# Kernel optimization log

Hardware: AMD Instinct MI355X
Metric: run time of the kernel (lower is better)

## Reference

```python
import jax, jax.numpy as jnp
import numpy as np
from jax import lax


def setup_inputs() -> dict:
    key = jax.random.key(0)
    t_in = jax.random.normal(key, (16, 65536, 3), dtype=jnp.float32)
    return {"npoints": 2048, "t_in": t_in}


def reference(npoints, t_in):
    """Iterative farthest point sampling.

    t_in: (b, n, 3) float32 point coordinates.
    Returns (b, npoints) int32 indices of sampled points.
    Matches the PointNet++ CUDA kernel semantics: first sample is index 0,
    running min-distance buffer initialized to a large value, each step
    picks the argmax of the min-distance to the already-selected set.
    """
    b, n, p = t_in.shape
    assert p == 3
    BIG = jnp.float32(1e10)

    batch_ix = jnp.arange(b)

    def step(carry, _):
        dist, last_idx = carry                      # dist: (b,n), last_idx: (b,)
        last = t_in[batch_ix, last_idx]             # (b,3) last selected points
        d = jnp.sum((t_in - last[:, None, :]) ** 2, axis=-1)  # (b,n)
        dist = jnp.minimum(dist, d)
        nxt = jnp.argmax(dist, axis=-1).astype(jnp.int32)      # (b,)
        return (dist, nxt), nxt

    init_idx = jnp.zeros((b,), dtype=jnp.int32)
    dist0 = jnp.full((b, n), BIG, dtype=jnp.float32)
    (_, _), idxs = lax.scan(step, (dist0, init_idx), None, length=npoints - 1)
    # idxs: (npoints-1, b) -> (b, npoints-1)
    out = jnp.concatenate([init_idx[:, None], idxs.T], axis=1)  # (b, npoints)
    return out
```

## Files before the change

kernel.cpp:

```cpp
#include <hip/hip_runtime.h>
#include <stdint.h>


#define NBATCH   16
#define NPTS     65536
#define NPOINTS  2048
#define KBLK     16
#define THREADS  256
#define WPB      64
#define PPB      4096
#define PPT      16
#define SLOT_U64 8
#define REGION_U64 (WPB * SLOT_U64)

#define TAGOK(w) (((unsigned)((w) >> 16) & 0xFFFFu) == tag)

typedef unsigned int uint4v __attribute__((ext_vector_type(4)));

__device__ __forceinline__ void load_slot16(const unsigned long long* p,
                                            unsigned long long& w0,
                                            unsigned long long& w1) {
    uint4v r;
    asm volatile("global_load_dwordx4 %0, %1, off sc0 sc1\n\t"
                 "s_waitcnt vmcnt(0)"
                 : "=v"(r) : "v"(p) : "memory");
    w0 = ((unsigned long long)r.y << 32) | r.x;
    w1 = ((unsigned long long)r.w << 32) | r.z;
}

__global__ __launch_bounds__(THREADS, 1)
void fps_kernel(const float* __restrict__ pts, int* __restrict__ out,
                unsigned long long* __restrict__ slots)
{
    const int bid  = blockIdx.x;
    const int g    = bid & 15;
    const int blk  = bid >> 4;
    const int tid  = threadIdx.x;
    const int lane = tid & 63;
    const int wave = tid >> 6;
    const int widx = (blk << 2) + wave;

    const float* __restrict__ P = pts + (size_t)g * (NPTS * 3);

    __shared__ unsigned long long s_flag[2];

    float  x[PPT], y[PPT], z[PPT];
    double dist[PPT];
    const int base = blk * PPB;
#pragma unroll
    for (int j = 0; j < PPT; ++j) {
        const int idx = base + j * THREADS + tid;
        x[j] = P[idx * 3 + 0];
        y[j] = P[idx * 3 + 1];
        z[j] = P[idx * 3 + 2];
        dist[j] = 1e10;
    }
    if (tid == 0) { s_flag[0] = 0ull; s_flag[1] = 0ull; }
    __syncthreads();

    double qx = (double)P[0], qy = (double)P[1], qz = (double)P[2];
    if (blk == 0 && tid == 0) out[g * NPOINTS] = 0;

    for (int it = 0; it < NPOINTS - 1; ++it) {
        double bd = -1.0;
        int    bi = 0x7FFFFFFF;
        {
#pragma clang fp contract(off)
#pragma unroll
            for (int j = 0; j < PPT; ++j) {
                const double dx = (double)x[j] - qx;
                const double dy = (double)y[j] - qy;
                const double dz = (double)z[j] - qz;
                const double d  = (dx * dx + dy * dy) + dz * dz;
                const double nd = fmin(dist[j], d);
                dist[j] = nd;
                const bool t = nd > bd;
                bd = t ? nd : bd;
                bi = t ? (base + j * THREADS + tid) : bi;
            }
        }

#pragma unroll
        for (int m = 1; m < 64; m <<= 1) {
            const double od = __shfl_xor(bd, m, 64);
            const int    oi = __shfl_xor(bi, m, 64);
            const bool t = (od > bd) || (od == bd && oi < bi);
            bd = t ? od : bd; bi = t ? oi : bi;
        }

        const unsigned tag = (unsigned)(it + 1);
        const int par = it & 1;
        unsigned long long* rb =
            slots + (size_t)(par * NBATCH + g) * REGION_U64;

        {
            const unsigned long long B =
                (unsigned long long)__double_as_longlong(bd);
            const unsigned long long TI =
                  ((unsigned long long)tag << 16)
                | (unsigned long long)((unsigned)bi & 0xFFFFu);
            const unsigned long long hi32 =
                (lane == 0) ? (B >> 32) : (B & 0xFFFFFFFFull);
            if (lane < 2) {
                __hip_atomic_store(rb + widx * SLOT_U64 + lane,
                                   (hi32 << 32) | TI,
                                   __ATOMIC_RELAXED, __HIP_MEMORY_SCOPE_AGENT);
            }
        }

        int wi;
        if (wave == 0) {
            unsigned long long* sp = rb + lane * SLOT_U64;
            __builtin_amdgcn_s_sleep(4);
            unsigned long long l0 = 0, l1 = 0;
            bool ok = false;
            int g1 = 0;
            do {
                load_slot16(sp, l0, l1);
                ok = TAGOK(l0) & TAGOK(l1);
            } while (!ok && ++g1 < 32);
            int g2 = 0;
            while (!ok) {
                l0 = __hip_atomic_load(sp + 0, __ATOMIC_RELAXED,
                                       __HIP_MEMORY_SCOPE_AGENT);
                l1 = __hip_atomic_load(sp + 1, __ATOMIC_RELAXED,
                                       __HIP_MEMORY_SCOPE_AGENT);
                ok = TAGOK(l0) & TAGOK(l1);
                if (++g2 > (1 << 20)) break;
            }

            double cd = __longlong_as_double(
                (long long)(((l0 >> 32) << 32) | (l1 >> 32)));
            int    ci = (int)(l0 & 0xFFFFull);

#pragma unroll
            for (int m = 1; m < 64; m <<= 1) {
                const double od = __shfl_xor(cd, m, 64);
                const int    oi = __shfl_xor(ci, m, 64);
                const bool t = (od > cd) || (od == cd && oi < ci);
                cd = t ? od : cd; ci = t ? oi : ci;
            }

            if (lane == 0) {
                __hip_atomic_store(&s_flag[par],
                                   ((unsigned long long)(unsigned)ci << 32)
                                 | (unsigned long long)tag,
                                   __ATOMIC_RELAXED,
                                   __HIP_MEMORY_SCOPE_WORKGROUP);
                if (blk == 0) out[g * NPOINTS + it + 1] = ci;
            }
            wi = ci;
        } else {
            unsigned long long fv;
            int guard = 0;
            do {
                fv = __hip_atomic_load(&s_flag[par], __ATOMIC_RELAXED,
                                       __HIP_MEMORY_SCOPE_WORKGROUP);
            } while (((unsigned)fv != tag) && ++guard < (1 << 20));
            wi = (int)(fv >> 32);
        }

        const float* pw = P + (size_t)(unsigned)wi * 3;
        qx = (double)pw[0]; qy = (double)pw[1]; qz = (double)pw[2];
    }
}

extern "C" void kernel_launch(void* const* d_in, const int* in_sizes, int n_in,
                              void* d_out, int out_size, void* d_ws, size_t ws_size,
                              hipStream_t stream) {
    (void)in_sizes; (void)n_in; (void)out_size; (void)ws_size;
    const float* t_in = (const float*)d_in[1];
    int* out = (int*)d_out;
    unsigned long long* slots = (unsigned long long*)d_ws;

    dim3 grid(NBATCH * KBLK);
    dim3 block(THREADS);
    void* args[] = { (void*)&t_in, (void*)&out, (void*)&slots };
    hipLaunchCooperativeKernel((const void*)fps_kernel, grid, block, args, 0, stream);
}
```

Before: 5.079 ms.

## Reduce per-block wave candidates in LDS before cross-block global exchange

Waves 1-3 now publish their per-wave best candidate to shared memory, and wave 0 merges them with its own before writing a single slot per block to global memory. The global exchange region shrinks from 64 wave slots to 16 block slots, so the poller reads fewer lines and runs a shorter shuffle reduction. In exchange, wave 0 must spin on LDS for the other waves before publishing, which adds a serial intra-block step to the critical path of every iteration.

Result: faster. 4.839 ms (-4.7%).

```diff
diff --git a/kernel.cpp b/kernel.cpp
--- a/kernel.cpp
+++ b/kernel.cpp
@@ -7,11 +7,10 @@
 #define NPOINTS  2048
 #define KBLK     16
 #define THREADS  256
-#define WPB      64
 #define PPB      4096
 #define PPT      16
 #define SLOT_U64 8
-#define REGION_U64 (WPB * SLOT_U64)
+#define REGION_U64 (KBLK * SLOT_U64)
 
 #define TAGOK(w) (((unsigned)((w) >> 16) & 0xFFFFu) == tag)
 
@@ -38,11 +37,11 @@
     const int tid  = threadIdx.x;
     const int lane = tid & 63;
     const int wave = tid >> 6;
-    const int widx = (blk << 2) + wave;
 
     const float* __restrict__ P = pts + (size_t)g * (NPTS * 3);
 
     __shared__ unsigned long long s_flag[2];
+    __shared__ unsigned long long s_cand[2][3][2];
 
     float  x[PPT], y[PPT], z[PPT];
     double dist[PPT];
@@ -55,7 +54,10 @@
         z[j] = P[idx * 3 + 2];
         dist[j] = 1e10;
     }
-    if (tid == 0) { s_flag[0] = 0ull; s_flag[1] = 0ull; }
+    if (tid < 16) {
+        ((unsigned long long*)s_cand)[tid & 11] = 0ull;
+        if (tid < 2) s_flag[tid] = 0ull;
+    }
     __syncthreads();
 
     double qx = (double)P[0], qy = (double)P[1], qz = (double)P[2];
@@ -93,24 +95,75 @@
         unsigned long long* rb =
             slots + (size_t)(par * NBATCH + g) * REGION_U64;
 
-        {
-            const unsigned long long B =
-                (unsigned long long)__double_as_longlong(bd);
-            const unsigned long long TI =
-                  ((unsigned long long)tag << 16)
-                | (unsigned long long)((unsigned)bi & 0xFFFFu);
-            const unsigned long long hi32 =
-                (lane == 0) ? (B >> 32) : (B & 0xFFFFFFFFull);
-            if (lane < 2) {
-                __hip_atomic_store(rb + widx * SLOT_U64 + lane,
-                                   (hi32 << 32) | TI,
-                                   __ATOMIC_RELAXED, __HIP_MEMORY_SCOPE_AGENT);
-            }
-        }
-
         int wi;
-        if (wave == 0) {
-            unsigned long long* sp = rb + lane * SLOT_U64;
+        if (wave != 0) {
+            if (lane == 0) {
+                const unsigned long long B =
+                    (unsigned long long)__double_as_longlong(bd);
+                const unsigned long long TI =
+                      ((unsigned long long)tag << 16)
+                    | (unsigned long long)((unsigned)bi & 0xFFFFu);
+                __hip_atomic_store(&s_cand[par][wave - 1][0],
+                                   ((B >> 32) << 32) | TI,
+                                   __ATOMIC_RELAXED,
+                                   __HIP_MEMORY_SCOPE_WORKGROUP);
+                __hip_atomic_store(&s_cand[par][wave - 1][1],
+                                   ((B & 0xFFFFFFFFull) << 32) | TI,
+                                   __ATOMIC_RELAXED,
+                                   __HIP_MEMORY_SCOPE_WORKGROUP);
+            }
+            unsigned long long fv;
+            int guard = 0;
+            do {
+                fv = __hip_atomic_load(&s_flag[par], __ATOMIC_RELAXED,
+                                       __HIP_MEMORY_SCOPE_WORKGROUP);
+            } while (((unsigned)fv != tag) && ++guard < (1 << 20));
+            wi = (int)(fv >> 32);
+        } else {
+            unsigned long long c[3][2];
+            {
+                int guard = 0;
+                bool all;
+                do {
+                    all = true;
+#pragma unroll
+                    for (int w = 0; w < 3; ++w) {
+                        c[w][0] = __hip_atomic_load(&s_cand[par][w][0],
+                                      __ATOMIC_RELAXED,
+                                      __HIP_MEMORY_SCOPE_WORKGROUP);
+                        c[w][1] = __hip_atomic_load(&s_cand[par][w][1],
+                                      __ATOMIC_RELAXED,
+                                      __HIP_MEMORY_SCOPE_WORKGROUP);
+                        all = all & TAGOK(c[w][0]) & TAGOK(c[w][1]);
+                    }
+                } while (!all && ++guard < (1 << 20));
+            }
+#pragma unroll
+            for (int w = 0; w < 3; ++w) {
+                const double od = __longlong_as_double((long long)(
+                    ((c[w][0] >> 32) << 32) | (c[w][1] >> 32)));
+                const int    oi = (int)(c[w][0] & 0xFFFFull);
+                const bool t = (od > bd) || (od == bd && oi < bi);
+                bd = t ? od : bd; bi = t ? oi : bi;
+            }
+
+            {
+                const unsigned long long B =
+                    (unsigned long long)__double_as_longlong(bd);
+                const unsigned long long TI =
+                      ((unsigned long long)tag << 16)
+                    | (unsigned long long)((unsigned)bi & 0xFFFFu);
+                const unsigned long long hi32 =
+                    (lane == 0) ? (B >> 32) : (B & 0xFFFFFFFFull);
+                if (lane < 2) {
+                    __hip_atomic_store(rb + blk * SLOT_U64 + lane,
+                                       (hi32 << 32) | TI,
+                                       __ATOMIC_RELAXED,
+                                       __HIP_MEMORY_SCOPE_AGENT);
+                }
+            }
+
+            unsigned long long* sp = rb + (lane & 15) * SLOT_U64;
             __builtin_amdgcn_s_sleep(4);
             unsigned long long l0 = 0, l1 = 0;
             bool ok = false;
@@ -134,7 +187,7 @@
             int    ci = (int)(l0 & 0xFFFFull);
 
 #pragma unroll
-            for (int m = 1; m < 64; m <<= 1) {
+            for (int m = 1; m < 16; m <<= 1) {
                 const double od = __shfl_xor(cd, m, 64);
                 const int    oi = __shfl_xor(ci, m, 64);
                 const bool t = (od > cd) || (od == cd && oi < ci);
@@ -150,14 +203,6 @@
                 if (blk == 0) out[g * NPOINTS + it + 1] = ci;
             }
             wi = ci;
-        } else {
-            unsigned long long fv;
-            int guard = 0;
-            do {
-                fv = __hip_atomic_load(&s_flag[par], __ATOMIC_RELAXED,
-                                       __HIP_MEMORY_SCOPE_WORKGROUP);
-            } while (((unsigned)fv != tag) && ++guard < (1 << 20));
-            wi = (int)(fv >> 32);
         }
 
         const float* pw = P + (size_t)(unsigned)wi * 3;
```
